# Performance work log

Hardware: AMD Instinct MI355X
Metric: run time of the kernel (lower is better)

## Reference

```python
import jax, jax.numpy as jnp
import numpy as np

BT, HID, E, INTER, TOPK = 256, 2048, 8, 4096, 2

def setup_inputs() -> dict:
    key = jax.random.key(0)
    k1, k2, k3, k4, k5 = jax.random.split(key, 5)
    hidden_states = jax.random.normal(k1, (BT, HID), dtype=jnp.float32)
    expert_routing_table = jax.random.randint(k2, (BT, TOPK), 0, E, dtype=jnp.int64)
    router_weights = jax.random.uniform(k3, (BT, TOPK), dtype=jnp.float32)
    # learned params, scaled like trained weights
    w13_weight = jax.random.normal(k4, (E, 2 * INTER, HID), dtype=jnp.float32) * 0.02
    w2_weight = jax.random.normal(k5, (E, HID, INTER), dtype=jnp.float32) * 0.02
    return {
        "hidden_states": hidden_states,
        "expert_routing_table": expert_routing_table,
        "router_weights": router_weights,
        "w13_weight": w13_weight,
        "w2_weight": w2_weight,
    }

def reference(hidden_states, expert_routing_table, router_weights, w13_weight, w2_weight):
    bt, hidden_dim = hidden_states.shape
    num_experts = w13_weight.shape[0]
    inter = w2_weight.shape[2]
    sel = expert_routing_table  # [bt, top_k], ep_shift = 0
    # scatter router weights into dense [bt, E] (torch scatter_ set semantics)
    rows = jnp.arange(bt)[:, None]
    padded_weights = jnp.zeros((bt, num_experts), dtype=hidden_states.dtype)
    padded_weights = padded_weights.at[rows, sel].set(router_weights)
    # dense per-expert up/gate projection: [bt, E, 2*inter]
    up_gate = jnp.einsum('th,efh->tef', hidden_states, w13_weight)
    up_gate = up_gate.reshape(bt, num_experts, 2, inter)
    up_states = up_gate[:, :, 0, :]
    gate_states = up_gate[:, :, 1, :]
    cur = jax.nn.silu(up_states) * gate_states  # [bt, E, inter]
    # down projection + masked routed-weight sum over experts
    down = jnp.einsum('tei,ehi->teh', cur, w2_weight)  # [bt, E, hidden]
    final = jnp.einsum('teh,te->th', down, padded_weights)
    return final.reshape(-1, hidden_dim)
```

## Files before the change

kernel.cpp:

```cpp
#include <hip/hip_runtime.h>

#define BT 256
#define HID 2048
#define NE 8
#define INTER 4096

typedef short short8 __attribute__((ext_vector_type(8)));
typedef float f32x4 __attribute__((ext_vector_type(4)));

__device__ inline unsigned short f2bf(float f){
  unsigned int u = __float_as_uint(f);
  u += 0x7fff + ((u >> 16) & 1);
  return (unsigned short)(u >> 16);
}
__device__ inline unsigned int pk2(float x, float y){
  return (unsigned int)f2bf(x) | ((unsigned int)f2bf(y) << 16);
}
__device__ inline short8 cvt8(float4 a, float4 b){
  union { unsigned int u[4]; short8 s; } r;
  r.u[0] = pk2(a.x, a.y); r.u[1] = pk2(a.z, a.w);
  r.u[2] = pk2(b.x, b.y); r.u[3] = pk2(b.z, b.w);
  return r.s;
}

__device__ inline void glds16(const void* g, void* l){
  __builtin_amdgcn_global_load_lds(
      (const __attribute__((address_space(1))) unsigned int*)g,
      (__attribute__((address_space(3))) unsigned int*)l, 16, 0, 0);
}

__device__ inline short8 fragf(const float* tile, int row, int kbase){
  int cp = (kbase >> 3) ^ (row & 7);
  const float4* p = (const float4*)(tile + row*64 + cp*8);
  return cvt8(p[0], p[1]);
}
__device__ inline short8 fragh(const unsigned short* tile, int row, int kbase){
  int cp = (kbase >> 3) ^ (row & 7);
  return *(const short8*)(tile + row*64 + cp*8);
}

__global__ void routing_kernel(const int* __restrict__ sel, const float* __restrict__ rw,
                               int* counts, int* bases, int* tokl, float* wtl){
  __shared__ int cnt[NE]; __shared__ int bs[NE]; __shared__ int cur[NE];
  int t = threadIdx.x;
  if (t < NE) cnt[t] = 0;
  __syncthreads();
  int s0 = sel[2*t], s1 = sel[2*t+1];
  float w0 = rw[2*t], w1 = rw[2*t+1];
  bool dup = (s0 == s1);
  atomicAdd(&cnt[s1], 1);
  if (!dup) atomicAdd(&cnt[s0], 1);
  __syncthreads();
  if (t == 0){ int a = 0; for (int e = 0; e < NE; e++){ bs[e] = a; cur[e] = a; a += cnt[e]; } }
  __syncthreads();
  int slot = atomicAdd(&cur[s1], 1); tokl[slot] = t; wtl[slot] = w1;
  if (!dup){ slot = atomicAdd(&cur[s0], 1); tokl[slot] = t; wtl[slot] = w0; }
  if (t < NE){ counts[t] = cnt[t]; bases[t] = bs[t]; }
}

__global__ __launch_bounds__(256, 3) void gemm1_kernel(
    const float* __restrict__ hs, const float* __restrict__ w13,
    const int* __restrict__ counts, const int* __restrict__ bases,
    const int* __restrict__ tokl, unsigned short* __restrict__ cur)
{
  const int e = blockIdx.z;
  const int cnt = counts[e];
  const int mtile = blockIdx.y;
  if (mtile * 64 >= cnt) return;
  const int f0 = blockIdx.x * 64;
  const int base = bases[e];
  const int tid = threadIdx.x;

  __shared__ __align__(16) float As[64*64];
  __shared__ __align__(16) float Bs[128*64];

  const float* gA[4]; int offA[4];
#pragma unroll
  for (int r = 0; r < 4; r++){
    int off = r*4096 + tid*16;
    int row = off >> 8, b = off & 255;
    int cp = b >> 5, half = (b >> 4) & 1;
    int col = ((cp ^ (row & 7)) * 8) + half*4;
    int slot = mtile*64 + row; if (slot >= cnt) slot = cnt - 1;
    gA[r] = hs + (size_t)tokl[base + slot] * HID + col;
    offA[r] = off;
  }
  const float* gB[8]; int offB[8];
#pragma unroll
  for (int r = 0; r < 8; r++){
    int off = r*4096 + tid*16;
    int row = off >> 8, b = off & 255;
    int cp = b >> 5, half = (b >> 4) & 1;
    int col = ((cp ^ (row & 7)) * 8) + half*4;
    int wrow = (row < 64) ? (f0 + row) : (INTER + f0 + row - 64);
    gB[r] = w13 + (size_t)e * 2*INTER*HID + (size_t)wrow * HID + col;
    offB[r] = off;
  }

  const int wv = tid >> 6, wm = wv >> 1, wn = wv & 1;
  const int lane = tid & 63;
  const int lrow = lane & 15, quad = lane >> 4;

  f32x4 acc[2][2][2];
#pragma unroll
  for (int s=0;s<2;s++) for (int mt=0;mt<2;mt++) for (int nt=0;nt<2;nt++)
    acc[s][mt][nt] = (f32x4){0.f,0.f,0.f,0.f};

  for (int k0 = 0; k0 < HID; k0 += 64){
#pragma unroll
    for (int r = 0; r < 4; r++) glds16(gA[r] + k0, (char*)As + offA[r]);
#pragma unroll
    for (int r = 0; r < 8; r++) glds16(gB[r] + k0, (char*)Bs + offB[r]);
    __syncthreads();
#pragma unroll
    for (int ks = 0; ks < 64; ks += 32){
      int kb = ks + quad*8;
      short8 a[2], bb[2][2];
#pragma unroll
      for (int mt=0;mt<2;mt++) a[mt] = fragf(As, wm*32 + mt*16 + lrow, kb);
#pragma unroll
      for (int s=0;s<2;s++)
#pragma unroll
        for (int nt=0;nt<2;nt++)
          bb[s][nt] = fragf(Bs, s*64 + wn*32 + nt*16 + lrow, kb);
#pragma unroll
      for (int s=0;s<2;s++)
#pragma unroll
        for (int mt=0;mt<2;mt++)
#pragma unroll
          for (int nt=0;nt<2;nt++)
            acc[s][mt][nt] = __builtin_amdgcn_mfma_f32_16x16x32_bf16(
                a[mt], bb[s][nt], acc[s][mt][nt], 0,0,0);
    }
    __syncthreads();
  }

#pragma unroll
  for (int mt = 0; mt < 2; mt++){
#pragma unroll
    for (int reg = 0; reg < 4; reg++){
      int m = mtile*64 + wm*32 + mt*16 + quad*4 + reg;
      if (m >= cnt) continue;
      size_t rowoff = (size_t)(base + m) * INTER;
#pragma unroll
      for (int nt = 0; nt < 2; nt++){
        int i = f0 + wn*32 + nt*16 + lrow;
        float up   = acc[0][mt][nt][reg];
        float gate = acc[1][mt][nt][reg];
        float sv = up / (1.f + __expf(-up));
        cur[rowoff + i] = f2bf(sv * gate);
      }
    }
  }
}

__global__ __launch_bounds__(256, 4) void gemm2_kernel(
    const unsigned short* __restrict__ cur, const float* __restrict__ w2,
    const int* __restrict__ counts, const int* __restrict__ bases,
    const int* __restrict__ tokl, const float* __restrict__ wtl,
    float* __restrict__ out)
{
  const int e  = blockIdx.z >> 1;
  const int kb0 = (blockIdx.z & 1) * 2048;
  const int cnt = counts[e];
  const int mtile = blockIdx.y;
  if (mtile * 64 >= cnt) return;
  const int h0 = blockIdx.x * 32;
  const int base = bases[e];
  const int tid = threadIdx.x;

  __shared__ __align__(16) unsigned short Ah[64*64];
  __shared__ __align__(16) float Bs[32*64];

  const unsigned short* gA[2]; int offA[2];
#pragma unroll
  for (int r = 0; r < 2; r++){
    int off = r*4096 + tid*16;
    int row = off >> 7;
    int cp = (off >> 4) & 7;
    int col = (cp ^ (row & 7)) * 8;
    int slot = mtile*64 + row; if (slot >= cnt) slot = cnt - 1;
    gA[r] = cur + (size_t)(base + slot) * INTER + kb0 + col;
    offA[r] = off;
  }
  const float* gB[2]; int offB[2];
#pragma unroll
  for (int r = 0; r < 2; r++){
    int off = r*4096 + tid*16;
    int row = off >> 8, b = off & 255;
    int cp = b >> 5, half = (b >> 4) & 1;
    int col = ((cp ^ (row & 7)) * 8) + half*4;
    gB[r] = w2 + (size_t)e * HID * INTER + (size_t)(h0 + row) * INTER + kb0 + col;
    offB[r] = off;
  }

  const int wv = tid >> 6, wm = wv >> 1, wn = wv & 1;
  const int lane = tid & 63;
  const int lrow = lane & 15, quad = lane >> 4;

  f32x4 acc[2];
  acc[0] = (f32x4){0.f,0.f,0.f,0.f};
  acc[1] = (f32x4){0.f,0.f,0.f,0.f};

  for (int k0 = 0; k0 < 2048; k0 += 64){
#pragma unroll
    for (int r = 0; r < 2; r++) glds16(gA[r] + k0, (char*)Ah + offA[r]);
#pragma unroll
    for (int r = 0; r < 2; r++) glds16(gB[r] + k0, (char*)Bs + offB[r]);
    __syncthreads();
#pragma unroll
    for (int ks = 0; ks < 64; ks += 32){
      int kb = ks + quad*8;
      short8 a[2], b;
#pragma unroll
      for (int mt=0;mt<2;mt++) a[mt] = fragh(Ah, wm*32 + mt*16 + lrow, kb);
      b = fragf(Bs, wn*16 + lrow, kb);
#pragma unroll
      for (int mt=0;mt<2;mt++)
        acc[mt] = __builtin_amdgcn_mfma_f32_16x16x32_bf16(a[mt], b, acc[mt], 0,0,0);
    }
    __syncthreads();
  }

#pragma unroll
  for (int mt = 0; mt < 2; mt++){
#pragma unroll
    for (int reg = 0; reg < 4; reg++){
      int m = mtile*64 + wm*32 + mt*16 + quad*4 + reg;
      if (m >= cnt) continue;
      int tk  = tokl[base + m];
      float w = wtl[base + m];
      int h = h0 + wn*16 + lrow;
      atomicAdd(&out[(size_t)tk * HID + h], w * acc[mt][reg]);
    }
  }
}

extern "C" void kernel_launch(void* const* d_in, const int* in_sizes, int n_in,
                              void* d_out, int out_size, void* d_ws, size_t ws_size,
                              hipStream_t stream){
  const float* hs  = (const float*)d_in[0];
  const int*   sel = (const int*)d_in[1];
  const float* rw  = (const float*)d_in[2];
  const float* w13 = (const float*)d_in[3];
  const float* w2  = (const float*)d_in[4];
  float* out = (float*)d_out;
  char* ws = (char*)d_ws;

  int* counts = (int*)ws;
  int* bases  = counts + 8;
  int* tokl   = bases + 8;
  float* wtl  = (float*)(tokl + 512);
  unsigned short* cur = (unsigned short*)(ws + 8192);

  hipMemsetAsync(d_out, 0, (size_t)BT * HID * sizeof(float), stream);
  routing_kernel<<<1, 256, 0, stream>>>(sel, rw, counts, bases, tokl, wtl);
  dim3 g1(INTER/64, 4, NE);
  gemm1_kernel<<<g1, 256, 0, stream>>>(hs, w13, counts, bases, tokl, cur);
  dim3 g2(HID/32, 4, NE*2);
  gemm2_kernel<<<g2, 256, 0, stream>>>(cur, w2, counts, bases, tokl, wtl, out);
}
```

Before: 925.4 us.

## Pre-gather bf16 activations, enlarge M tiles, and double-buffer both GEMMs

Adds a gather kernel that writes routed token rows as bf16 into a contiguous buffer, so gemm1 loads packed bf16 A tiles instead of converting fp32 per fragment. Both GEMMs move to 128-row M tiles with double-buffered LDS. Weights are loaded into registers one tile ahead, converted to bf16 and stored into the next buffer, overlapping loads with MFMA work. gemm2 drops its K split, halving atomic adds but leaving fewer blocks. The larger tiles and register prefetch lower occupancy, and the grids shrink, which may leave CUs idle given about 64 tokens per expert.

```diff
diff --git a/kernel.cpp b/kernel.cpp
--- a/kernel.cpp
+++ b/kernel.cpp
@@ -29,11 +29,6 @@
       (__attribute__((address_space(3))) unsigned int*)l, 16, 0, 0);
 }
 
-__device__ inline short8 fragf(const float* tile, int row, int kbase){
-  int cp = (kbase >> 3) ^ (row & 7);
-  const float4* p = (const float4*)(tile + row*64 + cp*8);
-  return cvt8(p[0], p[1]);
-}
 __device__ inline short8 fragh(const unsigned short* tile, int row, int kbase){
   int cp = (kbase >> 3) ^ (row & 7);
   return *(const short8*)(tile + row*64 + cp*8);
@@ -58,40 +53,53 @@
   if (t < NE){ counts[t] = cnt[t]; bases[t] = bs[t]; }
 }
 
-__global__ __launch_bounds__(256, 3) void gemm1_kernel(
-    const float* __restrict__ hs, const float* __restrict__ w13,
+__global__ void gather_kernel(const float* __restrict__ hs, const int* __restrict__ tokl,
+                              const int* __restrict__ counts, const int* __restrict__ bases,
+                              unsigned short* __restrict__ hsg){
+  int b = blockIdx.x;
+  int total = bases[NE-1] + counts[NE-1];
+  if (b >= total) return;
+  int tok = tokl[b];
+  const float4* src = (const float4*)(hs + (size_t)tok * HID);
+  short8* dst = (short8*)(hsg + (size_t)b * HID);
+  int t = threadIdx.x;
+  dst[t] = cvt8(src[2*t], src[2*t+1]);
+}
+
+__global__ __launch_bounds__(256, 2) void gemm1_kernel(
+    const unsigned short* __restrict__ hsg, const float* __restrict__ w13,
     const int* __restrict__ counts, const int* __restrict__ bases,
-    const int* __restrict__ tokl, unsigned short* __restrict__ cur)
+    unsigned short* __restrict__ cur)
 {
   const int e = blockIdx.z;
   const int cnt = counts[e];
   const int mtile = blockIdx.y;
-  if (mtile * 64 >= cnt) return;
+  if (mtile * 128 >= cnt) return;
   const int f0 = blockIdx.x * 64;
   const int base = bases[e];
   const int tid = threadIdx.x;
 
-  __shared__ __align__(16) float As[64*64];
-  __shared__ __align__(16) float Bs[128*64];
-
-  const float* gA[4]; int offA[4];
+  __shared__ __align__(16) unsigned short Ah[2][128*64];
+  __shared__ __align__(16) unsigned short Bh[2][128*64];
+
+  const unsigned short* gA[4]; int offA[4];
 #pragma unroll
   for (int r = 0; r < 4; r++){
     int off = r*4096 + tid*16;
-    int row = off >> 8, b = off & 255;
-    int cp = b >> 5, half = (b >> 4) & 1;
-    int col = ((cp ^ (row & 7)) * 8) + half*4;
-    int slot = mtile*64 + row; if (slot >= cnt) slot = cnt - 1;
-    gA[r] = hs + (size_t)tokl[base + slot] * HID + col;
+    int row = off >> 7;
+    int cp  = (off >> 4) & 7;
+    int col = (cp ^ (row & 7)) * 8;
+    int slot = mtile*128 + row; if (slot >= cnt) slot = cnt - 1;
+    gA[r] = hsg + (size_t)(base + slot) * HID + col;
     offA[r] = off;
   }
-  const float* gB[8]; int offB[8];
-#pragma unroll
-  for (int r = 0; r < 8; r++){
+  const float* gB[4]; int offB[4];
+#pragma unroll
+  for (int r = 0; r < 4; r++){
     int off = r*4096 + tid*16;
-    int row = off >> 8, b = off & 255;
-    int cp = b >> 5, half = (b >> 4) & 1;
-    int col = ((cp ^ (row & 7)) * 8) + half*4;
+    int row = off >> 7;
+    int cp  = (off >> 4) & 7;
+    int col = (cp ^ (row & 7)) * 8;
     int wrow = (row < 64) ? (f0 + row) : (INTER + f0 + row - 64);
     gB[r] = w13 + (size_t)e * 2*INTER*HID + (size_t)wrow * HID + col;
     offB[r] = off;
@@ -101,52 +109,78 @@
   const int lane = tid & 63;
   const int lrow = lane & 15, quad = lane >> 4;
 
-  f32x4 acc[2][2][2];
-#pragma unroll
-  for (int s=0;s<2;s++) for (int mt=0;mt<2;mt++) for (int nt=0;nt<2;nt++)
-    acc[s][mt][nt] = (f32x4){0.f,0.f,0.f,0.f};
-
-  for (int k0 = 0; k0 < HID; k0 += 64){
-#pragma unroll
-    for (int r = 0; r < 4; r++) glds16(gA[r] + k0, (char*)As + offA[r]);
-#pragma unroll
-    for (int r = 0; r < 8; r++) glds16(gB[r] + k0, (char*)Bs + offB[r]);
-    __syncthreads();
+  f32x4 acc[2][4][2];
+#pragma unroll
+  for (int s=0;s<2;s++)
+#pragma unroll
+    for (int mf=0;mf<4;mf++)
+#pragma unroll
+      for (int nt=0;nt<2;nt++) acc[s][mf][nt] = (f32x4){0.f,0.f,0.f,0.f};
+
+  float4 bv[4][2];
+#pragma unroll
+  for (int r = 0; r < 4; r++) glds16(gA[r], (char*)Ah[0] + offA[r]);
+#pragma unroll
+  for (int r = 0; r < 4; r++){ bv[r][0] = *(const float4*)(gB[r]); bv[r][1] = *(const float4*)(gB[r] + 4); }
+#pragma unroll
+  for (int r = 0; r < 4; r++) *(short8*)((char*)Bh[0] + offB[r]) = cvt8(bv[r][0], bv[r][1]);
+  asm volatile("s_waitcnt vmcnt(0) lgkmcnt(0)" ::: "memory");
+  __builtin_amdgcn_s_barrier();
+  __builtin_amdgcn_sched_barrier(0);
+
+  int cb = 0;
+  for (int t = 0; t < HID/64; ++t){
+    const int nb = cb ^ 1;
+    const bool pf = (t + 1 < HID/64);
+    const int kn = (t + 1) * 64;
+    if (pf){
+#pragma unroll
+      for (int r = 0; r < 4; r++) glds16(gA[r] + kn, (char*)Ah[nb] + offA[r]);
+#pragma unroll
+      for (int r = 0; r < 4; r++){ bv[r][0] = *(const float4*)(gB[r] + kn); bv[r][1] = *(const float4*)(gB[r] + kn + 4); }
+    }
 #pragma unroll
     for (int ks = 0; ks < 64; ks += 32){
-      int kb = ks + quad*8;
-      short8 a[2], bb[2][2];
-#pragma unroll
-      for (int mt=0;mt<2;mt++) a[mt] = fragf(As, wm*32 + mt*16 + lrow, kb);
+      const int kb = ks + quad*8;
+      short8 a[4], b[2][2];
+#pragma unroll
+      for (int mf=0;mf<4;mf++) a[mf] = fragh(Ah[cb], wm*64 + mf*16 + lrow, kb);
 #pragma unroll
       for (int s=0;s<2;s++)
 #pragma unroll
         for (int nt=0;nt<2;nt++)
-          bb[s][nt] = fragf(Bs, s*64 + wn*32 + nt*16 + lrow, kb);
+          b[s][nt] = fragh(Bh[cb], s*64 + wn*32 + nt*16 + lrow, kb);
 #pragma unroll
       for (int s=0;s<2;s++)
 #pragma unroll
-        for (int mt=0;mt<2;mt++)
+        for (int mf=0;mf<4;mf++)
 #pragma unroll
           for (int nt=0;nt<2;nt++)
-            acc[s][mt][nt] = __builtin_amdgcn_mfma_f32_16x16x32_bf16(
-                a[mt], bb[s][nt], acc[s][mt][nt], 0,0,0);
-    }
-    __syncthreads();
-  }
-
-#pragma unroll
-  for (int mt = 0; mt < 2; mt++){
+            acc[s][mf][nt] = __builtin_amdgcn_mfma_f32_16x16x32_bf16(
+                a[mf], b[s][nt], acc[s][mf][nt], 0,0,0);
+    }
+    if (pf){
+#pragma unroll
+      for (int r = 0; r < 4; r++) *(short8*)((char*)Bh[nb] + offB[r]) = cvt8(bv[r][0], bv[r][1]);
+    }
+    asm volatile("s_waitcnt vmcnt(0) lgkmcnt(0)" ::: "memory");
+    __builtin_amdgcn_s_barrier();
+    __builtin_amdgcn_sched_barrier(0);
+    cb = nb;
+  }
+
+#pragma unroll
+  for (int mf = 0; mf < 4; mf++){
 #pragma unroll
     for (int reg = 0; reg < 4; reg++){
-      int m = mtile*64 + wm*32 + mt*16 + quad*4 + reg;
+      int m = mtile*128 + wm*64 + mf*16 + quad*4 + reg;
       if (m >= cnt) continue;
       size_t rowoff = (size_t)(base + m) * INTER;
 #pragma unroll
       for (int nt = 0; nt < 2; nt++){
         int i = f0 + wn*32 + nt*16 + lrow;
-        float up   = acc[0][mt][nt][reg];
-        float gate = acc[1][mt][nt][reg];
+        float up   = acc[0][mf][nt][reg];
+        float gate = acc[1][mf][nt][reg];
         float sv = up / (1.f + __expf(-up));
         cur[rowoff + i] = f2bf(sv * gate);
       }
@@ -154,84 +188,99 @@
   }
 }
 
-__global__ __launch_bounds__(256, 4) void gemm2_kernel(
+__global__ __launch_bounds__(256, 3) void gemm2_kernel(
     const unsigned short* __restrict__ cur, const float* __restrict__ w2,
     const int* __restrict__ counts, const int* __restrict__ bases,
     const int* __restrict__ tokl, const float* __restrict__ wtl,
     float* __restrict__ out)
 {
-  const int e  = blockIdx.z >> 1;
-  const int kb0 = (blockIdx.z & 1) * 2048;
+  const int e = blockIdx.z;
   const int cnt = counts[e];
   const int mtile = blockIdx.y;
-  if (mtile * 64 >= cnt) return;
+  if (mtile * 128 >= cnt) return;
   const int h0 = blockIdx.x * 32;
   const int base = bases[e];
   const int tid = threadIdx.x;
 
-  __shared__ __align__(16) unsigned short Ah[64*64];
-  __shared__ __align__(16) float Bs[32*64];
-
-  const unsigned short* gA[2]; int offA[2];
-#pragma unroll
-  for (int r = 0; r < 2; r++){
+  __shared__ __align__(16) unsigned short Ah[2][128*64];
+  __shared__ __align__(16) unsigned short Bh[2][32*64];
+
+  const unsigned short* gA[4]; int offA[4];
+#pragma unroll
+  for (int r = 0; r < 4; r++){
     int off = r*4096 + tid*16;
     int row = off >> 7;
-    int cp = (off >> 4) & 7;
+    int cp  = (off >> 4) & 7;
     int col = (cp ^ (row & 7)) * 8;
-    int slot = mtile*64 + row; if (slot >= cnt) slot = cnt - 1;
-    gA[r] = cur + (size_t)(base + slot) * INTER + kb0 + col;
+    int slot = mtile*128 + row; if (slot >= cnt) slot = cnt - 1;
+    gA[r] = cur + (size_t)(base + slot) * INTER + col;
     offA[r] = off;
   }
-  const float* gB[2]; int offB[2];
-#pragma unroll
-  for (int r = 0; r < 2; r++){
-    int off = r*4096 + tid*16;
-    int row = off >> 8, b = off & 255;
-    int cp = b >> 5, half = (b >> 4) & 1;
-    int col = ((cp ^ (row & 7)) * 8) + half*4;
-    gB[r] = w2 + (size_t)e * HID * INTER + (size_t)(h0 + row) * INTER + kb0 + col;
-    offB[r] = off;
+  const float* gB; int offB;
+  {
+    int off = tid*16;
+    int row = off >> 7;
+    int cp  = (off >> 4) & 7;
+    int col = (cp ^ (row & 7)) * 8;
+    gB = w2 + (size_t)e * HID * INTER + (size_t)(h0 + row) * INTER + col;
+    offB = off;
   }
 
   const int wv = tid >> 6, wm = wv >> 1, wn = wv & 1;
   const int lane = tid & 63;
   const int lrow = lane & 15, quad = lane >> 4;
 
-  f32x4 acc[2];
-  acc[0] = (f32x4){0.f,0.f,0.f,0.f};
-  acc[1] = (f32x4){0.f,0.f,0.f,0.f};
-
-  for (int k0 = 0; k0 < 2048; k0 += 64){
-#pragma unroll
-    for (int r = 0; r < 2; r++) glds16(gA[r] + k0, (char*)Ah + offA[r]);
-#pragma unroll
-    for (int r = 0; r < 2; r++) glds16(gB[r] + k0, (char*)Bs + offB[r]);
-    __syncthreads();
+  f32x4 acc[4];
+#pragma unroll
+  for (int mf=0;mf<4;mf++) acc[mf] = (f32x4){0.f,0.f,0.f,0.f};
+
+  float4 bv0, bv1;
+#pragma unroll
+  for (int r = 0; r < 4; r++) glds16(gA[r], (char*)Ah[0] + offA[r]);
+  bv0 = *(const float4*)gB; bv1 = *(const float4*)(gB + 4);
+  *(short8*)((char*)Bh[0] + offB) = cvt8(bv0, bv1);
+  asm volatile("s_waitcnt vmcnt(0) lgkmcnt(0)" ::: "memory");
+  __builtin_amdgcn_s_barrier();
+  __builtin_amdgcn_sched_barrier(0);
+
+  int cb = 0;
+  for (int t = 0; t < INTER/64; ++t){
+    const int nb = cb ^ 1;
+    const bool pf = (t + 1 < INTER/64);
+    const int kn = (t + 1) * 64;
+    if (pf){
+#pragma unroll
+      for (int r = 0; r < 4; r++) glds16(gA[r] + kn, (char*)Ah[nb] + offA[r]);
+      bv0 = *(const float4*)(gB + kn); bv1 = *(const float4*)(gB + kn + 4);
+    }
 #pragma unroll
     for (int ks = 0; ks < 64; ks += 32){
-      int kb = ks + quad*8;
-      short8 a[2], b;
-#pragma unroll
-      for (int mt=0;mt<2;mt++) a[mt] = fragh(Ah, wm*32 + mt*16 + lrow, kb);
-      b = fragf(Bs, wn*16 + lrow, kb);
-#pragma unroll
-      for (int mt=0;mt<2;mt++)
-        acc[mt] = __builtin_amdgcn_mfma_f32_16x16x32_bf16(a[mt], b, acc[mt], 0,0,0);
-    }
-    __syncthreads();
-  }
-
-#pragma unroll
-  for (int mt = 0; mt < 2; mt++){
+      const int kb = ks + quad*8;
+      short8 a[4], b;
+#pragma unroll
+      for (int mf=0;mf<4;mf++) a[mf] = fragh(Ah[cb], wm*64 + mf*16 + lrow, kb);
+      b = fragh(Bh[cb], wn*16 + lrow, kb);
+#pragma unroll
+      for (int mf=0;mf<4;mf++)
+        acc[mf] = __builtin_amdgcn_mfma_f32_16x16x32_bf16(a[mf], b, acc[mf], 0,0,0);
+    }
+    if (pf) *(short8*)((char*)Bh[nb] + offB) = cvt8(bv0, bv1);
+    asm volatile("s_waitcnt vmcnt(0) lgkmcnt(0)" ::: "memory");
+    __builtin_amdgcn_s_barrier();
+    __builtin_amdgcn_sched_barrier(0);
+    cb = nb;
+  }
+
+#pragma unroll
+  for (int mf = 0; mf < 4; mf++){
 #pragma unroll
     for (int reg = 0; reg < 4; reg++){
-      int m = mtile*64 + wm*32 + mt*16 + quad*4 + reg;
+      int m = mtile*128 + wm*64 + mf*16 + quad*4 + reg;
       if (m >= cnt) continue;
       int tk  = tokl[base + m];
       float w = wtl[base + m];
       int h = h0 + wn*16 + lrow;
-      atomicAdd(&out[(size_t)tk * HID + h], w * acc[mt][reg]);
+      atomicAdd(&out[(size_t)tk * HID + h], w * acc[mf][reg]);
     }
   }
 }
@@ -251,12 +300,14 @@
   int* bases  = counts + 8;
   int* tokl   = bases + 8;
   float* wtl  = (float*)(tokl + 512);
-  unsigned short* cur = (unsigned short*)(ws + 8192);
+  unsigned short* hsg = (unsigned short*)(ws + 8192);
+  unsigned short* cur = (unsigned short*)(ws + 8192 + (size_t)512*HID*2);
 
   hipMemsetAsync(d_out, 0, (size_t)BT * HID * sizeof(float), stream);
   routing_kernel<<<1, 256, 0, stream>>>(sel, rw, counts, bases, tokl, wtl);
-  dim3 g1(INTER/64, 4, NE);
-  gemm1_kernel<<<g1, 256, 0, stream>>>(hs, w13, counts, bases, tokl, cur);
-  dim3 g2(HID/32, 4, NE*2);
+  gather_kernel<<<512, 256, 0, stream>>>(hs, tokl, counts, bases, hsg);
+  dim3 g1(INTER/64, 2, NE);
+  gemm1_kernel<<<g1, 256, 0, stream>>>(hsg, w13, counts, bases, cur);
+  dim3 g2(HID/32, 2, NE);
   gemm2_kernel<<<g2, 256, 0, stream>>>(cur, w2, counts, bases, tokl, wtl, out);
 }
```

Result: slower. 951.4 us (+2.8%).
